# Optimization experiments

Measured on AMD Instinct MI355X. Metric: run time of the kernel, lower is better.

The kernel has to match this reference:

```python
import jax, jax.numpy as jnp
import numpy as np

N_NODES = 100000

def gin_conv(x, edge_index, W, b):
    # PyG GINConv with eps=0: out = Linear(x + sum_{j->i} x_j)
    src, dst = edge_index[0], edge_index[1]
    agg = jax.ops.segment_sum(x[src], dst, num_segments=N_NODES)  # [N, d]
    return (x + agg) @ W + b

def setup_inputs() -> dict:
    key = jax.random.key(0)
    ks = jax.random.split(key, 8)
    x = jax.random.normal(ks[0], (N_NODES, 32), dtype=jnp.float32)
    edge_index = jax.random.randint(ks[1], (2, 1600000), 0, N_NODES, dtype=jnp.int64)
    def lin(k, fan_in, fan_out):
        kw, kb = jax.random.split(k)
        lim = 1.0 / np.sqrt(fan_in)
        W = jax.random.uniform(kw, (fan_in, fan_out), minval=-lim, maxval=lim, dtype=jnp.float32)
        b = jax.random.uniform(kb, (fan_out,), minval=-lim, maxval=lim, dtype=jnp.float32)
        return W, b
    W1, b1 = lin(ks[2], 32, 64)
    W2, b2 = lin(ks[3], 64, 64)
    W3, b3 = lin(ks[4], 64, 10)
    return {"x": x, "edge_index": edge_index,
            "W1": W1, "b1": b1, "W2": W2, "b2": b2, "W3": W3, "b3": b3}

def reference(x, edge_index, W1, b1, W2, b2, W3, b3):
    h = jax.nn.relu(gin_conv(x, edge_index, W1, b1))
    h = jax.nn.relu(gin_conv(h, edge_index, W2, b2))
    return gin_conv(h, edge_index, W3, b3)  # [N, classes] logits
```

## Files before the change

kernel.cpp:

```cpp
#include <hip/hip_runtime.h>


#define GIN_N 100000
#define NBUCKET 256
#define NB2 391
#define BSTRIDE 8192
#define EPT 16

typedef unsigned short bfu;
typedef float v2f __attribute__((ext_vector_type(2)));

__device__ __forceinline__ float bf_lo(unsigned int u) {
    return __uint_as_float(u << 16);
}
__device__ __forceinline__ float bf_hi(unsigned int u) {
    return __uint_as_float(u & 0xffff0000u);
}
__device__ __forceinline__ v2f bf_v2(unsigned int u) {
    return v2f{bf_lo(u), bf_hi(u)};
}
__device__ __forceinline__ unsigned int f2bf(float f) {
    unsigned int u = __float_as_uint(f);
    return (u + 0x7fffu + ((u >> 16) & 1u)) >> 16;
}
__device__ __forceinline__ v2f fp8lo(unsigned u) {
    return __builtin_amdgcn_cvt_pk_f32_fp8(u, false);
}
__device__ __forceinline__ v2f fp8hi(unsigned u) {
    return __builtin_amdgcn_cvt_pk_f32_fp8(u, true);
}

template <int S>
__device__ __forceinline__ void blelloch_excl(int* a) {
#pragma unroll
    for (int d = 1; d < S; d <<= 1) {
        __syncthreads();
        int idx = (threadIdx.x + 1) * (d << 1) - 1;
        if (idx < S) a[idx] += a[idx - d];
    }
    __syncthreads();
    if (threadIdx.x == 0) a[S - 1] = 0;
#pragma unroll
    for (int d = S >> 1; d >= 1; d >>= 1) {
        __syncthreads();
        int idx = (threadIdx.x + 1) * (d << 1) - 1;
        if (idx < S) {
            int t = a[idx - d];
            a[idx - d] = a[idx];
            a[idx] += t;
        }
    }
    __syncthreads();
}

__global__ __launch_bounds__(256) void build_kernel(
        const int* __restrict__ src, const int* __restrict__ dst, int E,
        unsigned* __restrict__ bucketbuf, int* __restrict__ cursor,
        const float* __restrict__ x, unsigned* __restrict__ xq, int n8,
        int bblk) {
    __shared__ int h[NBUCKET];
    __shared__ int base[NBUCKET];
    int tid = threadIdx.x;
    if (blockIdx.x >= bblk) {
        int t = (blockIdx.x - bblk) * 256 + tid;
        if (t >= n8) return;
        const float4* v = reinterpret_cast<const float4*>(x);
        float4 a = v[2 * t], b = v[2 * t + 1];
        unsigned w0 = 0, w1 = 0;
        w0 = __builtin_amdgcn_cvt_pk_fp8_f32(a.x, a.y, w0, false);
        w0 = __builtin_amdgcn_cvt_pk_fp8_f32(a.z, a.w, w0, true);
        w1 = __builtin_amdgcn_cvt_pk_fp8_f32(b.x, b.y, w1, false);
        w1 = __builtin_amdgcn_cvt_pk_fp8_f32(b.z, b.w, w1, true);
        reinterpret_cast<uint2*>(xq)[t] = make_uint2(w0, w1);
        return;
    }
    int chunk0 = blockIdx.x * (256 * EPT);
    h[tid] = 0;
    __syncthreads();
    int myb[EPT];
    unsigned myrec[EPT];
#pragma unroll
    for (int i = 0; i < EPT; ++i) {
        int e = chunk0 + tid + i * 256;
        if (e < E) {
            int d = dst[e];
            int s = src[e];
            int b = d / NB2;
            myb[i] = b;
            myrec[i] = ((unsigned)(d - b * NB2) << 17) | (unsigned)s;
            atomicAdd(&h[b], 1);
        } else {
            myb[i] = -1;
        }
    }
    __syncthreads();
    base[tid] = atomicAdd(&cursor[tid], h[tid]);
    h[tid] = 0;
    __syncthreads();
#pragma unroll
    for (int i = 0; i < EPT; ++i) {
        int b = myb[i];
        if (b < 0) continue;
        int pos = base[b] + atomicAdd(&h[b], 1);
        if (pos < BSTRIDE) bucketbuf[(size_t)b * BSTRIDE + pos] = myrec[i];
    }
}

__global__ __launch_bounds__(256) void csr_build_kernel(
        const unsigned* __restrict__ bucketbuf,
        const int* __restrict__ cursor,
        int* __restrict__ rowptr,
        int* __restrict__ adj) {
    __shared__ int csr[BSTRIDE];
    __shared__ int cnt[512];
    __shared__ int off[512];
    __shared__ int bscan[NBUCKET];
    int b = blockIdx.x;
    int tid = threadIdx.x;
    bscan[tid] = cursor[tid];
    int mycnt = cursor[b];
    if (mycnt > BSTRIDE) mycnt = BSTRIDE;
    blelloch_excl<NBUCKET>(bscan);
    int base = bscan[b];

    const unsigned* buf = bucketbuf + (size_t)b * BSTRIDE;
    cnt[tid] = 0;
    cnt[tid + 256] = 0;
    __syncthreads();
    for (int i = tid; i < mycnt; i += 256)
        atomicAdd(&cnt[buf[i] >> 17], 1);
    __syncthreads();
    off[tid] = cnt[tid];
    off[tid + 256] = cnt[tid + 256];
    blelloch_excl<512>(off);

    int nodes0 = b * NB2;
    int nn2 = GIN_N + 1 - nodes0;
    if (nn2 > NB2) nn2 = NB2;
    for (int l = tid; l < nn2; l += 256) rowptr[nodes0 + l] = base + off[l];
    __syncthreads();

    for (int i = tid; i < mycnt; i += 256) {
        unsigned r = buf[i];
        int pos = atomicAdd(&off[r >> 17], 1);
        csr[pos] = (int)(r & 0x1FFFFu);
    }
    __syncthreads();
    for (int i = tid; i < mycnt; i += 256) adj[base + i] = csr[i];
}

__global__ __launch_bounds__(256, 8) void fused1_kernel(
        const float* __restrict__ xf,
        const unsigned* __restrict__ xq,
        const int* __restrict__ rowptr,
        const int* __restrict__ adj,
        const float* __restrict__ W,
        const float* __restrict__ b,
        unsigned* __restrict__ outq) {
    constexpr int K = 32, M = 64;
    constexpr int TPN = 4, NODES = 64, TP2 = 4, MT = 16;
    constexpr int STR = K + 4;

    __shared__ unsigned Wp[K * M / 2];
    __shared__ float bs[M];
    __shared__ float tile[NODES * STR];

    for (int i = threadIdx.x; i < K * M / 2; i += 256) {
        float w0 = W[2 * i], w1 = W[2 * i + 1];
        Wp[i] = f2bf(w0) | (f2bf(w1) << 16);
    }
    if (threadIdx.x < M) bs[threadIdx.x] = b[threadIdx.x];
    __syncthreads();

    int node0 = blockIdx.x * NODES;
    int tid = threadIdx.x;
    int l = tid / TPN;
    int n = node0 + l;

    if (n < GIN_N) {
        int j = tid % TPN;
        int start = rowptr[n];
        int d = rowptr[n + 1] - start;
        const int* row = adj + start;
        const uint2* fq = reinterpret_cast<const uint2*>(xq);
        v2f a0, a1, a2, a3;
        {
            const float4* xv = reinterpret_cast<const float4*>(xf);
            float4 a = xv[(size_t)n * 8 + 2 * j];
            float4 c = xv[(size_t)n * 8 + 2 * j + 1];
            a0 = v2f{a.x, a.y}; a1 = v2f{a.z, a.w};
            a2 = v2f{c.x, c.y}; a3 = v2f{c.z, c.w};
        }
#define ACC8(v) { a0 += fp8lo(v.x); a1 += fp8hi(v.x); \
                  a2 += fp8lo(v.y); a3 += fp8hi(v.y); }
        int k = 0;
        for (; k + 8 <= d; k += 8) {
            uint2 v0 = fq[(size_t)row[k] * 4 + j];
            uint2 v1 = fq[(size_t)row[k + 1] * 4 + j];
            uint2 v2 = fq[(size_t)row[k + 2] * 4 + j];
            uint2 v3 = fq[(size_t)row[k + 3] * 4 + j];
            uint2 v4 = fq[(size_t)row[k + 4] * 4 + j];
            uint2 v5 = fq[(size_t)row[k + 5] * 4 + j];
            uint2 v6 = fq[(size_t)row[k + 6] * 4 + j];
            uint2 v7 = fq[(size_t)row[k + 7] * 4 + j];
            ACC8(v0) ACC8(v1) ACC8(v2) ACC8(v3)
            ACC8(v4) ACC8(v5) ACC8(v6) ACC8(v7)
        }
        for (; k + 4 <= d; k += 4) {
            uint2 v0 = fq[(size_t)row[k] * 4 + j];
            uint2 v1 = fq[(size_t)row[k + 1] * 4 + j];
            uint2 v2 = fq[(size_t)row[k + 2] * 4 + j];
            uint2 v3 = fq[(size_t)row[k + 3] * 4 + j];
            ACC8(v0) ACC8(v1) ACC8(v2) ACC8(v3)
        }
        for (; k < d; ++k) {
            uint2 v = fq[(size_t)row[k] * 4 + j];
            ACC8(v)
        }
#undef ACC8
        float* tp = &tile[l * STR + j * 8];
        tp[0] = a0.x; tp[1] = a0.y; tp[2] = a1.x; tp[3] = a1.y;
        tp[4] = a2.x; tp[5] = a2.y; tp[6] = a3.x; tp[7] = a3.y;
    }
    __builtin_amdgcn_wave_barrier();

    if (n < GIN_N) {
        int sub = tid % TP2;
        float acc[MT];
#pragma unroll
        for (int jj = 0; jj < MT; ++jj) acc[jj] = bs[sub * MT + jj];
        const float* tp = &tile[l * STR];
#pragma unroll
        for (int k = 0; k < K; ++k) {
            float v = tp[k];
            const unsigned* wr = &Wp[k * (M / 2) + sub * (MT / 2)];
#pragma unroll
            for (int j2 = 0; j2 < MT / 2; ++j2) {
                unsigned wp = wr[j2];
                acc[2 * j2]     = fmaf(v, bf_lo(wp), acc[2 * j2]);
                acc[2 * j2 + 1] = fmaf(v, bf_hi(wp), acc[2 * j2 + 1]);
            }
        }
#pragma unroll
        for (int jj = 0; jj < MT; ++jj) acc[jj] = fmaxf(acc[jj], 0.0f);
        unsigned q[4];
#pragma unroll
        for (int q4 = 0; q4 < 4; ++q4) {
            unsigned w = 0;
            w = __builtin_amdgcn_cvt_pk_fp8_f32(acc[4 * q4], acc[4 * q4 + 1], w, false);
            w = __builtin_amdgcn_cvt_pk_fp8_f32(acc[4 * q4 + 2], acc[4 * q4 + 3], w, true);
            q[q4] = w;
        }
        reinterpret_cast<uint4*>(outq)[(size_t)n * 4 + sub] =
            make_uint4(q[0], q[1], q[2], q[3]);
    }
}

__global__ __launch_bounds__(256, 8) void fused2t_kernel(
        const unsigned* __restrict__ xq,
        const int* __restrict__ rowptr,
        const int* __restrict__ adj,
        const float* __restrict__ W,
        const float* __restrict__ b,
        const float* __restrict__ W3,
        unsigned* __restrict__ tout) {
    constexpr int K = 64, M = 64;
    constexpr int TPN = 8, NODES = 32, TP2 = 8, MT = 8;
    constexpr int STR = K + 4;

    __shared__ unsigned Wp[K * M / 2];
    __shared__ float bs[M];
    __shared__ float W3t[10 * K];
    __shared__ float tile[NODES * STR];

    for (int i = threadIdx.x; i < K * M / 2; i += 256) {
        float w0 = W[2 * i], w1 = W[2 * i + 1];
        Wp[i] = f2bf(w0) | (f2bf(w1) << 16);
    }
    for (int i = threadIdx.x; i < 10 * K; i += 256) {
        int jj = i >> 6, k = i & 63;
        W3t[i] = W3[k * 10 + jj];
    }
    if (threadIdx.x < M) bs[threadIdx.x] = b[threadIdx.x];
    __syncthreads();

    int node0 = blockIdx.x * NODES;
    int tid = threadIdx.x;
    int l = tid / TPN;
    int n = node0 + l;

    if (n < GIN_N) {
        int j = tid % TPN;
        int start = rowptr[n];
        int d = rowptr[n + 1] - start;
        const int* row = adj + start;
        const uint2* fq = reinterpret_cast<const uint2*>(xq);
        v2f a0, a1, a2, a3;
        {
            uint2 s = fq[(size_t)n * 8 + j];
            a0 = fp8lo(s.x); a1 = fp8hi(s.x);
            a2 = fp8lo(s.y); a3 = fp8hi(s.y);
        }
#define ACC8(v) { a0 += fp8lo(v.x); a1 += fp8hi(v.x); \
                  a2 += fp8lo(v.y); a3 += fp8hi(v.y); }
        int k = 0;
        for (; k + 8 <= d; k += 8) {
            uint2 v0 = fq[(size_t)row[k] * 8 + j];
            uint2 v1 = fq[(size_t)row[k + 1] * 8 + j];
            uint2 v2 = fq[(size_t)row[k + 2] * 8 + j];
            uint2 v3 = fq[(size_t)row[k + 3] * 8 + j];
            uint2 v4 = fq[(size_t)row[k + 4] * 8 + j];
            uint2 v5 = fq[(size_t)row[k + 5] * 8 + j];
            uint2 v6 = fq[(size_t)row[k + 6] * 8 + j];
            uint2 v7 = fq[(size_t)row[k + 7] * 8 + j];
            ACC8(v0) ACC8(v1) ACC8(v2) ACC8(v3)
            ACC8(v4) ACC8(v5) ACC8(v6) ACC8(v7)
        }
        for (; k + 4 <= d; k += 4) {
            uint2 v0 = fq[(size_t)row[k] * 8 + j];
            uint2 v1 = fq[(size_t)row[k + 1] * 8 + j];
            uint2 v2 = fq[(size_t)row[k + 2] * 8 + j];
            uint2 v3 = fq[(size_t)row[k + 3] * 8 + j];
            ACC8(v0) ACC8(v1) ACC8(v2) ACC8(v3)
        }
        for (; k < d; ++k) {
            uint2 v = fq[(size_t)row[k] * 8 + j];
            ACC8(v)
        }
#undef ACC8
        float* tp = &tile[l * STR + j * 8];
        tp[0] = a0.x; tp[1] = a0.y; tp[2] = a1.x; tp[3] = a1.y;
        tp[4] = a2.x; tp[5] = a2.y; tp[6] = a3.x; tp[7] = a3.y;
    }
    __builtin_amdgcn_wave_barrier();

    if (n < GIN_N) {
        int sub = tid % TP2;
        float acc[MT];
#pragma unroll
        for (int jj = 0; jj < MT; ++jj) acc[jj] = bs[sub * MT + jj];
        const float* tp = &tile[l * STR];
#pragma unroll
        for (int k = 0; k < K; ++k) {
            float v = tp[k];
            const unsigned* wr = &Wp[k * (M / 2) + sub * (MT / 2)];
#pragma unroll
            for (int j2 = 0; j2 < MT / 2; ++j2) {
                unsigned wp = wr[j2];
                acc[2 * j2]     = fmaf(v, bf_lo(wp), acc[2 * j2]);
                acc[2 * j2 + 1] = fmaf(v, bf_hi(wp), acc[2 * j2 + 1]);
            }
        }
#pragma unroll
        for (int jj = 0; jj < MT; ++jj) acc[jj] = fmaxf(acc[jj], 0.0f);
        float pt[10];
#pragma unroll
        for (int jj = 0; jj < 10; ++jj) {
            const float* wr = &W3t[jj * K + sub * MT];
            float v = acc[0] * wr[0];
#pragma unroll
            for (int kk = 1; kk < MT; ++kk) v = fmaf(acc[kk], wr[kk], v);
            pt[jj] = v;
        }
#pragma unroll
        for (int jj = 0; jj < 10; ++jj) {
            float v = pt[jj];
            v += __shfl_xor(v, 1, 64);
            v += __shfl_xor(v, 2, 64);
            v += __shfl_xor(v, 4, 64);
            pt[jj] = v;
        }
        if (sub == 0) {
            unsigned p[8];
#pragma unroll
            for (int j2 = 0; j2 < 5; ++j2)
                p[j2] = f2bf(pt[2 * j2]) | (f2bf(pt[2 * j2 + 1]) << 16);
            p[5] = 0; p[6] = 0; p[7] = 0;
            uint4* o = reinterpret_cast<uint4*>(tout) + (size_t)n * 2;
            o[0] = make_uint4(p[0], p[1], p[2], p[3]);
            o[1] = make_uint4(p[4], p[5], p[6], p[7]);
        }
    }
}

__global__ __launch_bounds__(256, 8) void gather_final_kernel(
        const unsigned* __restrict__ t8,
        const int* __restrict__ rowptr,
        const int* __restrict__ adj,
        const float* __restrict__ b3,
        float* __restrict__ out) {
    int t = blockIdx.x * blockDim.x + threadIdx.x;
    int n = t >> 1;
    int j = t & 1;
    if (n >= GIN_N) return;
    int start = rowptr[n];
    int d = rowptr[n + 1] - start;
    const int* row = adj + start;
    const uint4* T = reinterpret_cast<const uint4*>(t8);
    v2f a[4];
    {
        uint4 s = T[(size_t)n * 2 + j];
        a[0] = bf_v2(s.x); a[1] = bf_v2(s.y);
        a[2] = bf_v2(s.z); a[3] = bf_v2(s.w);
    }
#define ACC_T(v) \
    a[0] += bf_v2(v.x); a[1] += bf_v2(v.y); \
    a[2] += bf_v2(v.z); a[3] += bf_v2(v.w);
    int k = 0;
    for (; k + 8 <= d; k += 8) {
        uint4 v0 = T[(size_t)row[k] * 2 + j];
        uint4 v1 = T[(size_t)row[k + 1] * 2 + j];
        uint4 v2 = T[(size_t)row[k + 2] * 2 + j];
        uint4 v3 = T[(size_t)row[k + 3] * 2 + j];
        uint4 v4 = T[(size_t)row[k + 4] * 2 + j];
        uint4 v5 = T[(size_t)row[k + 5] * 2 + j];
        uint4 v6 = T[(size_t)row[k + 6] * 2 + j];
        uint4 v7 = T[(size_t)row[k + 7] * 2 + j];
        ACC_T(v0) ACC_T(v1) ACC_T(v2) ACC_T(v3)
        ACC_T(v4) ACC_T(v5) ACC_T(v6) ACC_T(v7)
    }
    for (; k < d; ++k) {
        uint4 v = T[(size_t)row[k] * 2 + j];
        ACC_T(v)
    }
#undef ACC_T
    float* o = out + (size_t)n * 10 + j * 8;
    if (j == 0) {
        const float2* b2v = reinterpret_cast<const float2*>(b3);
#pragma unroll
        for (int c = 0; c < 4; ++c) {
            float2 bb = b2v[c];
            reinterpret_cast<float2*>(o)[c] =
                make_float2(a[c].x + bb.x, a[c].y + bb.y);
        }
    } else {
        reinterpret_cast<float2*>(o)[0] =
            make_float2(a[0].x + b3[8], a[0].y + b3[9]);
    }
}

extern "C" void kernel_launch(void* const* d_in, const int* in_sizes, int n_in,
                              void* d_out, int out_size, void* d_ws, size_t ws_size,
                              hipStream_t stream) {
    const float* x  = (const float*)d_in[0];
    const int*   ei = (const int*)d_in[1];
    const float* W1 = (const float*)d_in[2];
    const float* b1 = (const float*)d_in[3];
    const float* W2 = (const float*)d_in[4];
    const float* b2 = (const float*)d_in[5];
    const float* W3 = (const float*)d_in[6];
    const float* b3 = (const float*)d_in[7];
    float* out = (float*)d_out;

    const int N = GIN_N;
    const int E = in_sizes[1] / 2;
    const int* src = ei;
    const int* dst = ei + E;

    unsigned* Xq = (unsigned*)d_ws;
    unsigned* H1q = Xq + (size_t)N * 8;
    unsigned* Tb = H1q + (size_t)N * 16;
    int* rowptr = (int*)(Tb + (size_t)N * 8);
    int* cursor = rowptr + (N + 8);
    int* adj = cursor + 256;
    unsigned* bucketbuf = (unsigned*)(adj + (size_t)E);

    const int BLK = 256;

    hipMemsetAsync(cursor, 0, 256 * sizeof(int), stream);
    {
        int n8 = N * 32 / 8;
        int bblk = (E + BLK * EPT - 1) / (BLK * EPT);
        int xblk = (n8 + BLK - 1) / BLK;
        build_kernel<<<bblk + xblk, BLK, 0, stream>>>(
            src, dst, E, bucketbuf, cursor, x, Xq, n8, bblk);
        csr_build_kernel<<<NBUCKET, BLK, 0, stream>>>(
            bucketbuf, cursor, rowptr, adj);
    }

    fused1_kernel<<<(N + 63) / 64, BLK, 0, stream>>>(
        x, Xq, rowptr, adj, W1, b1, H1q);

    fused2t_kernel<<<(N + 31) / 32, BLK, 0, stream>>>(
        H1q, rowptr, adj, W2, b2, W3, Tb);

    gather_final_kernel<<<(N * 2 + BLK - 1) / BLK, BLK, 0, stream>>>(
        Tb, rowptr, adj, b3, out);
}
```

Baseline: 204.8 us.

## Widen gather loads to 16 bytes per lane and store bf16 tiles in LDS

Both fused gather+linear kernels now have each lane fetch 16 fp8 features (uint4) per neighbor instead of 8. That halves the threads per node and doubles the nodes per block. The aggregated tile is packed to bf16 pairs in shared memory, halving LDS footprint and reads. The matmul then processes two k values per packed word. In fused1, the aggregation and transform phases now use different thread-to-node mappings (2 vs 4 lanes per node), so a full __syncthreads and a two-pass transform were added. Fewer lanes per node means fewer concurrent gather streams per node and extra bf16 rounding of the aggregate before the matmul.

Result: slower. 280.0 us (+36.7%).

```diff
diff --git a/kernel.cpp b/kernel.cpp
--- a/kernel.cpp
+++ b/kernel.cpp
@@ -28,6 +28,12 @@
 }
 __device__ __forceinline__ v2f fp8hi(unsigned u) {
     return __builtin_amdgcn_cvt_pk_f32_fp8(u, true);
+}
+__device__ __forceinline__ void acc_fp8x16(v2f* a, uint4 v) {
+    a[0] += fp8lo(v.x); a[1] += fp8hi(v.x);
+    a[2] += fp8lo(v.y); a[3] += fp8hi(v.y);
+    a[4] += fp8lo(v.z); a[5] += fp8hi(v.z);
+    a[6] += fp8lo(v.w); a[7] += fp8hi(v.w);
 }
 
 template <int S>
@@ -158,12 +164,12 @@
         const float* __restrict__ b,
         unsigned* __restrict__ outq) {
     constexpr int K = 32, M = 64;
-    constexpr int TPN = 4, NODES = 64, TP2 = 4, MT = 16;
-    constexpr int STR = K + 4;
+    constexpr int NODES = 128, MT = 16;
+    constexpr int STRU = 20;
 
     __shared__ unsigned Wp[K * M / 2];
     __shared__ float bs[M];
-    __shared__ float tile[NODES * STR];
+    __shared__ unsigned tileu[NODES * STRU];
 
     for (int i = threadIdx.x; i < K * M / 2; i += 256) {
         float w0 = W[2 * i], w1 = W[2 * i + 1];
@@ -174,71 +180,68 @@
 
     int node0 = blockIdx.x * NODES;
     int tid = threadIdx.x;
-    int l = tid / TPN;
-    int n = node0 + l;
-
-    if (n < GIN_N) {
-        int j = tid % TPN;
-        int start = rowptr[n];
-        int d = rowptr[n + 1] - start;
-        const int* row = adj + start;
-        const uint2* fq = reinterpret_cast<const uint2*>(xq);
-        v2f a0, a1, a2, a3;
-        {
-            const float4* xv = reinterpret_cast<const float4*>(xf);
-            float4 a = xv[(size_t)n * 8 + 2 * j];
-            float4 c = xv[(size_t)n * 8 + 2 * j + 1];
-            a0 = v2f{a.x, a.y}; a1 = v2f{a.z, a.w};
-            a2 = v2f{c.x, c.y}; a3 = v2f{c.z, c.w};
-        }
-#define ACC8(v) { a0 += fp8lo(v.x); a1 += fp8hi(v.x); \
-                  a2 += fp8lo(v.y); a3 += fp8hi(v.y); }
-        int k = 0;
-        for (; k + 8 <= d; k += 8) {
-            uint2 v0 = fq[(size_t)row[k] * 4 + j];
-            uint2 v1 = fq[(size_t)row[k + 1] * 4 + j];
-            uint2 v2 = fq[(size_t)row[k + 2] * 4 + j];
-            uint2 v3 = fq[(size_t)row[k + 3] * 4 + j];
-            uint2 v4 = fq[(size_t)row[k + 4] * 4 + j];
-            uint2 v5 = fq[(size_t)row[k + 5] * 4 + j];
-            uint2 v6 = fq[(size_t)row[k + 6] * 4 + j];
-            uint2 v7 = fq[(size_t)row[k + 7] * 4 + j];
-            ACC8(v0) ACC8(v1) ACC8(v2) ACC8(v3)
-            ACC8(v4) ACC8(v5) ACC8(v6) ACC8(v7)
-        }
-        for (; k + 4 <= d; k += 4) {
-            uint2 v0 = fq[(size_t)row[k] * 4 + j];
-            uint2 v1 = fq[(size_t)row[k + 1] * 4 + j];
-            uint2 v2 = fq[(size_t)row[k + 2] * 4 + j];
-            uint2 v3 = fq[(size_t)row[k + 3] * 4 + j];
-            ACC8(v0) ACC8(v1) ACC8(v2) ACC8(v3)
-        }
-        for (; k < d; ++k) {
-            uint2 v = fq[(size_t)row[k] * 4 + j];
-            ACC8(v)
-        }
-#undef ACC8
-        float* tp = &tile[l * STR + j * 8];
-        tp[0] = a0.x; tp[1] = a0.y; tp[2] = a1.x; tp[3] = a1.y;
-        tp[4] = a2.x; tp[5] = a2.y; tp[6] = a3.x; tp[7] = a3.y;
-    }
-    __builtin_amdgcn_wave_barrier();
-
-    if (n < GIN_N) {
-        int sub = tid % TP2;
+
+    {
+        int l = tid >> 1;
+        int j = tid & 1;
+        int n = node0 + l;
+        if (n < GIN_N) {
+            int start = rowptr[n];
+            int d = rowptr[n + 1] - start;
+            const int* row = adj + start;
+            const uint4* fq4 = reinterpret_cast<const uint4*>(xq);
+            v2f a[8];
+            {
+                const float4* xv = reinterpret_cast<const float4*>(xf);
+#pragma unroll
+                for (int c = 0; c < 4; ++c) {
+                    float4 s = xv[(size_t)n * 8 + j * 4 + c];
+                    a[2 * c] = v2f{s.x, s.y};
+                    a[2 * c + 1] = v2f{s.z, s.w};
+                }
+            }
+            int k = 0;
+            for (; k + 4 <= d; k += 4) {
+                uint4 v0 = fq4[(size_t)row[k] * 2 + j];
+                uint4 v1 = fq4[(size_t)row[k + 1] * 2 + j];
+                uint4 v2 = fq4[(size_t)row[k + 2] * 2 + j];
+                uint4 v3 = fq4[(size_t)row[k + 3] * 2 + j];
+                acc_fp8x16(a, v0); acc_fp8x16(a, v1);
+                acc_fp8x16(a, v2); acc_fp8x16(a, v3);
+            }
+            for (; k < d; ++k) acc_fp8x16(a, fq4[(size_t)row[k] * 2 + j]);
+            unsigned* tp = &tileu[l * STRU + j * 8];
+#pragma unroll
+            for (int q = 0; q < 8; ++q)
+                tp[q] = f2bf(a[q].x) | (f2bf(a[q].y) << 16);
+        }
+    }
+    __syncthreads();
+
+#pragma unroll
+    for (int pass = 0; pass < 2; ++pass) {
+        int l = pass * 64 + (tid >> 2);
+        int sub = tid & 3;
+        int n = node0 + l;
+        if (n >= GIN_N) continue;
         float acc[MT];
 #pragma unroll
         for (int jj = 0; jj < MT; ++jj) acc[jj] = bs[sub * MT + jj];
-        const float* tp = &tile[l * STR];
-#pragma unroll
-        for (int k = 0; k < K; ++k) {
-            float v = tp[k];
-            const unsigned* wr = &Wp[k * (M / 2) + sub * (MT / 2)];
+        const unsigned* tpu = &tileu[l * STRU];
+#pragma unroll
+        for (int k2 = 0; k2 < K / 2; ++k2) {
+            unsigned u = tpu[k2];
+            float v0 = bf_lo(u), v1 = bf_hi(u);
+            const unsigned* wr0 = &Wp[(2 * k2) * (M / 2) + sub * (MT / 2)];
+            const unsigned* wr1 = &Wp[(2 * k2 + 1) * (M / 2) + sub * (MT / 2)];
 #pragma unroll
             for (int j2 = 0; j2 < MT / 2; ++j2) {
-                unsigned wp = wr[j2];
-                acc[2 * j2]     = fmaf(v, bf_lo(wp), acc[2 * j2]);
-                acc[2 * j2 + 1] = fmaf(v, bf_hi(wp), acc[2 * j2 + 1]);
+                unsigned wp0 = wr0[j2];
+                acc[2 * j2]     = fmaf(v0, bf_lo(wp0), acc[2 * j2]);
+                acc[2 * j2 + 1] = fmaf(v0, bf_hi(wp0), acc[2 * j2 + 1]);
+                unsigned wp1 = wr1[j2];
+                acc[2 * j2]     = fmaf(v1, bf_lo(wp1), acc[2 * j2]);
+                acc[2 * j2 + 1] = fmaf(v1, bf_hi(wp1), acc[2 * j2 + 1]);
             }
         }
 #pragma unroll
@@ -265,13 +268,13 @@
         const float* __restrict__ W3,
         unsigned* __restrict__ tout) {
     constexpr int K = 64, M = 64;
-    constexpr int TPN = 8, NODES = 32, TP2 = 8, MT = 8;
-    constexpr int STR = K + 4;
+    constexpr int NODES = 64, MT = 16;
+    constexpr int STRU = 36;
 
     __shared__ unsigned Wp[K * M / 2];
     __shared__ float bs[M];
     __shared__ float W3t[10 * K];
-    __shared__ float tile[NODES * STR];
+    __shared__ unsigned tileu[NODES * STRU];
 
     for (int i = threadIdx.x; i < K * M / 2; i += 256) {
         float w0 = W[2 * i], w1 = W[2 * i + 1];
@@ -286,69 +289,59 @@
 
     int node0 = blockIdx.x * NODES;
     int tid = threadIdx.x;
-    int l = tid / TPN;
+    int l = tid >> 2;
     int n = node0 + l;
 
     if (n < GIN_N) {
-        int j = tid % TPN;
+        int j = tid & 3;
         int start = rowptr[n];
         int d = rowptr[n + 1] - start;
         const int* row = adj + start;
-        const uint2* fq = reinterpret_cast<const uint2*>(xq);
-        v2f a0, a1, a2, a3;
+        const uint4* fq4 = reinterpret_cast<const uint4*>(xq);
+        v2f a[8];
         {
-            uint2 s = fq[(size_t)n * 8 + j];
-            a0 = fp8lo(s.x); a1 = fp8hi(s.x);
-            a2 = fp8lo(s.y); a3 = fp8hi(s.y);
-        }
-#define ACC8(v) { a0 += fp8lo(v.x); a1 += fp8hi(v.x); \
-                  a2 += fp8lo(v.y); a3 += fp8hi(v.y); }
+            uint4 s = fq4[(size_t)n * 4 + j];
+#pragma unroll
+            for (int q = 0; q < 8; ++q) a[q] = v2f{0.f, 0.f};
+            acc_fp8x16(a, s);
+        }
         int k = 0;
-        for (; k + 8 <= d; k += 8) {
-            uint2 v0 = fq[(size_t)row[k] * 8 + j];
-            uint2 v1 = fq[(size_t)row[k + 1] * 8 + j];
-            uint2 v2 = fq[(size_t)row[k + 2] * 8 + j];
-            uint2 v3 = fq[(size_t)row[k + 3] * 8 + j];
-            uint2 v4 = fq[(size_t)row[k + 4] * 8 + j];
-            uint2 v5 = fq[(size_t)row[k + 5] * 8 + j];
-            uint2 v6 = fq[(size_t)row[k + 6] * 8 + j];
-            uint2 v7 = fq[(size_t)row[k + 7] * 8 + j];
-            ACC8(v0) ACC8(v1) ACC8(v2) ACC8(v3)
-            ACC8(v4) ACC8(v5) ACC8(v6) ACC8(v7)
-        }
         for (; k + 4 <= d; k += 4) {
-            uint2 v0 = fq[(size_t)row[k] * 8 + j];
-            uint2 v1 = fq[(size_t)row[k + 1] * 8 + j];
-            uint2 v2 = fq[(size_t)row[k + 2] * 8 + j];
-            uint2 v3 = fq[(size_t)row[k + 3] * 8 + j];
-            ACC8(v0) ACC8(v1) ACC8(v2) ACC8(v3)
-        }
-        for (; k < d; ++k) {
-            uint2 v = fq[(size_t)row[k] * 8 + j];
-            ACC8(v)
-        }
-#undef ACC8
-        float* tp = &tile[l * STR + j * 8];
-        tp[0] = a0.x; tp[1] = a0.y; tp[2] = a1.x; tp[3] = a1.y;
-        tp[4] = a2.x; tp[5] = a2.y; tp[6] = a3.x; tp[7] = a3.y;
+            uint4 v0 = fq4[(size_t)row[k] * 4 + j];
+            uint4 v1 = fq4[(size_t)row[k + 1] * 4 + j];
+            uint4 v2 = fq4[(size_t)row[k + 2] * 4 + j];
+            uint4 v3 = fq4[(size_t)row[k + 3] * 4 + j];
+            acc_fp8x16(a, v0); acc_fp8x16(a, v1);
+            acc_fp8x16(a, v2); acc_fp8x16(a, v3);
+        }
+        for (; k < d; ++k) acc_fp8x16(a, fq4[(size_t)row[k] * 4 + j]);
+        unsigned* tp = &tileu[l * STRU + (tid & 3) * 8];
+#pragma unroll
+        for (int q = 0; q < 8; ++q)
+            tp[q] = f2bf(a[q].x) | (f2bf(a[q].y) << 16);
     }
     __builtin_amdgcn_wave_barrier();
 
     if (n < GIN_N) {
-        int sub = tid % TP2;
+        int sub = tid & 3;
         float acc[MT];
 #pragma unroll
         for (int jj = 0; jj < MT; ++jj) acc[jj] = bs[sub * MT + jj];
-        const float* tp = &tile[l * STR];
-#pragma unroll
-        for (int k = 0; k < K; ++k) {
-            float v = tp[k];
-            const unsigned* wr = &Wp[k * (M / 2) + sub * (MT / 2)];
+        const unsigned* tpu = &tileu[l * STRU];
+#pragma unroll
+        for (int k2 = 0; k2 < K / 2; ++k2) {
+            unsigned u = tpu[k2];
+            float v0 = bf_lo(u), v1 = bf_hi(u);
+            const unsigned* wr0 = &Wp[(2 * k2) * (M / 2) + sub * (MT / 2)];
+            const unsigned* wr1 = &Wp[(2 * k2 + 1) * (M / 2) + sub * (MT / 2)];
 #pragma unroll
             for (int j2 = 0; j2 < MT / 2; ++j2) {
-                unsigned wp = wr[j2];
-                acc[2 * j2]     = fmaf(v, bf_lo(wp), acc[2 * j2]);
-                acc[2 * j2 + 1] = fmaf(v, bf_hi(wp), acc[2 * j2 + 1]);
+                unsigned wp0 = wr0[j2];
+                acc[2 * j2]     = fmaf(v0, bf_lo(wp0), acc[2 * j2]);
+                acc[2 * j2 + 1] = fmaf(v0, bf_hi(wp0), acc[2 * j2 + 1]);
+                unsigned wp1 = wr1[j2];
+                acc[2 * j2]     = fmaf(v1, bf_lo(wp1), acc[2 * j2]);
+                acc[2 * j2 + 1] = fmaf(v1, bf_hi(wp1), acc[2 * j2 + 1]);
             }
         }
 #pragma unroll
@@ -367,7 +360,6 @@
             float v = pt[jj];
             v += __shfl_xor(v, 1, 64);
             v += __shfl_xor(v, 2, 64);
-            v += __shfl_xor(v, 4, 64);
             pt[jj] = v;
         }
         if (sub == 0) {
@@ -478,10 +470,10 @@
             bucketbuf, cursor, rowptr, adj);
     }
 
-    fused1_kernel<<<(N + 63) / 64, BLK, 0, stream>>>(
+    fused1_kernel<<<(N + 127) / 128, BLK, 0, stream>>>(
         x, Xq, rowptr, adj, W1, b1, H1q);
 
-    fused2t_kernel<<<(N + 31) / 32, BLK, 0, stream>>>(
+    fused2t_kernel<<<(N + 63) / 64, BLK, 0, stream>>>(
         H1q, rowptr, adj, W2, b2, W3, Tb);
 
     gather_final_kernel<<<(N * 2 + BLK - 1) / BLK, BLK, 0, stream>>>(
```
